# Optimization experiments

Measured on AMD Instinct MI355X. Metric: run time of the kernel, lower is better.

The kernel has to match this reference:

```python
import jax, jax.numpy as jnp
import numpy as np

NEI_SIZE = [16]  # matches init kwarg nei_size

def setup_inputs() -> dict:
    key = jax.random.key(0)
    k = jax.random.split(key, 5)
    B, N, S = 512, 32, 16
    EF, NF = 64, 128
    return {
        "x": jax.random.normal(k[0], (B, N, NF), dtype=jnp.float32),
        "x_nei_rel": jax.random.normal(k[1], (B, N * S, EF), dtype=jnp.float32),
        "x_nei_node": jax.random.normal(k[2], (B, N * S, NF), dtype=jnp.float32),
        "W1_w": jax.random.normal(k[3], (NF, EF + NF), dtype=jnp.float32) * 0.05,
        "W1_b": jax.random.normal(k[4], (NF,), dtype=jnp.float32) * 0.05,
        "i": 0,
    }

def reference(x, x_nei_rel, x_nei_node, W1_w, W1_b, i):
    S = NEI_SIZE[i]                       # now_nei_size (static python int)
    B, N, D = x.shape                     # N = n_neibor, D = nodeFea
    norm = 1.0 / np.sqrt(D).astype(np.float32)
    # concat edge+node feats and project: [B, N*S, EF+NF] -> [B, N*S, D]
    x_nei = jnp.concatenate([x_nei_rel, x_nei_node], axis=-1)
    v = (x_nei @ W1_w.T + W1_b).reshape(B, N, S, D)
    # per-node attention over its S neighbors
    alpha = jnp.einsum('bnd,bnsd->bns', x, v) * norm   # [B, N, S]
    alpha = jax.nn.softmax(alpha, axis=-1)
    # weighted neighbor sum
    return jnp.einsum('bns,bnsd->bnd', alpha, v)       # [B, N, D]
```

## Files before the change

### kernel.cpp

```cpp
#include <hip/hip_runtime.h>
#include <stdint.h>


typedef __attribute__((ext_vector_type(8))) short short8;
typedef __attribute__((ext_vector_type(4))) float float4_t;
typedef __attribute__((ext_vector_type(4))) unsigned short ushort4_t;

#define GRID_ 1024
#define ITERS_ 8

__device__ __forceinline__ unsigned short f2bf(float f) {
    uint32_t u = __float_as_uint(f);
    u += 0x7fffu + ((u >> 16) & 1u);
    return (unsigned short)(u >> 16);
}

__device__ __forceinline__ int aoff(int s, int kc) {
    return (((kc >> 5) * 64) + (((kc & 31) >> 3) * 16) + s) * 8 + (kc & 7);
}

__global__ __launch_bounds__(512, 8) void nei_attn_kernel(
    const float* __restrict__ x,
    const float* __restrict__ rel,
    const float* __restrict__ node,
    const float* __restrict__ W,
    const float* __restrict__ bias,
    float* __restrict__ out)
{
    __shared__ __align__(16) unsigned short lds_a[2][6 * 64 * 8];
    __shared__ float lds_x[2][128];
    __shared__ float lds_v[2][16 * 132];
    __shared__ float lds_alpha[2][16];

    const int t    = threadIdx.x;
    const int tl   = t & 255;
    const int h    = t >> 8;
    const int lane = t & 63;
    const int wv   = t >> 6;
    const int l15  = lane & 15;
    const int quad = (lane >> 4) & 3;

    short8 bf[6];
    const int row = wv * 16 + l15;
    const float bias_c = bias[row];
    #pragma unroll
    for (int q = 0; q < 6; ++q) {
        const float* p = W + row * 192 + q * 32 + quad * 8;
        float4_t a0 = *(const float4_t*)p;
        float4_t a1 = *(const float4_t*)(p + 4);
        short8 f;
        f[0] = (short)f2bf(a0.x); f[1] = (short)f2bf(a0.y);
        f[2] = (short)f2bf(a0.z); f[3] = (short)f2bf(a0.w);
        f[4] = (short)f2bf(a1.x); f[5] = (short)f2bf(a1.y);
        f[6] = (short)f2bf(a1.z); f[7] = (short)f2bf(a1.w);
        bf[q] = f;
    }

    const int s0 = tl >> 4,  kc0 = (tl & 15) << 2;
    const int s1 = tl >> 5,  kc1 = 64 + ((tl & 31) << 2);
    const int s2 = s1 + 8;
    const int ao0 = h * 3072 + aoff(s0, kc0);
    const int ao1 = h * 3072 + aoff(s1, kc1);
    const int ao2 = h * 3072 + aoff(s2, kc1);
    unsigned short* la = &lds_a[0][0];

    int idx = blockIdx.x * (ITERS_ * 2);

    float4_t pf0, pf1, pf2;
    float pfx = 0.f;
    {
        const float* pr = rel  + (idx + h) * 1024;
        const float* pn = node + (idx + h) * 2048;
        pf0 = *(const float4_t*)(pr + tl * 4);
        pf1 = *(const float4_t*)(pn + tl * 4);
        pf2 = *(const float4_t*)(pn + 1024 + tl * 4);
        if (t < 256) pfx = x[(idx + (t >> 7)) * 128 + (t & 127)];
    }

    for (int it = 0; it < ITERS_; ++it) {
        {
            ushort4_t u;
            u[0] = f2bf(pf0.x); u[1] = f2bf(pf0.y); u[2] = f2bf(pf0.z); u[3] = f2bf(pf0.w);
            *(ushort4_t*)&la[ao0] = u;
            u[0] = f2bf(pf1.x); u[1] = f2bf(pf1.y); u[2] = f2bf(pf1.z); u[3] = f2bf(pf1.w);
            *(ushort4_t*)&la[ao1] = u;
            u[0] = f2bf(pf2.x); u[1] = f2bf(pf2.y); u[2] = f2bf(pf2.z); u[3] = f2bf(pf2.w);
            *(ushort4_t*)&la[ao2] = u;
            if (t < 256) lds_x[t >> 7][t & 127] = pfx;
        }
        __syncthreads();

        if (it + 1 < ITERS_) {
            const int nidx = idx + 2;
            const float* pr = rel  + (nidx + h) * 1024;
            const float* pn = node + (nidx + h) * 2048;
            pf0 = *(const float4_t*)(pr + tl * 4);
            pf1 = *(const float4_t*)(pn + tl * 4);
            pf2 = *(const float4_t*)(pn + 1024 + tl * 4);
            if (t < 256) pfx = x[(nidx + (t >> 7)) * 128 + (t & 127)];
        }

        float4_t acc0 = {0.f, 0.f, 0.f, 0.f};
        float4_t acc1 = {0.f, 0.f, 0.f, 0.f};
        #pragma unroll
        for (int q = 0; q < 6; ++q) {
            short8 af0 = *(const short8*)&la[(q * 64 + lane) * 8];
            short8 af1 = *(const short8*)&la[3072 + (q * 64 + lane) * 8];
            acc0 = __builtin_amdgcn_mfma_f32_16x16x32_bf16(af0, bf[q], acc0, 0, 0, 0);
            acc1 = __builtin_amdgcn_mfma_f32_16x16x32_bf16(af1, bf[q], acc1, 0, 0, 0);
        }
        const int colw = wv * 16 + l15;
        const int rb = quad * 4;
        #pragma unroll
        for (int r = 0; r < 4; ++r) {
            lds_v[0][(rb + r) * 132 + colw] = acc0[r] + bias_c;
            lds_v[1][(rb + r) * 132 + colw] = acc1[r] + bias_c;
        }
        __syncthreads();

        {
            const int sA = tl >> 4, dA = tl & 15;
            float p = 0.f;
            #pragma unroll
            for (int j = 0; j < 8; ++j) {
                const int d = dA + (j << 4);
                p += lds_x[h][d] * lds_v[h][sA * 132 + d];
            }
            p += __shfl_xor(p, 8);
            p += __shfl_xor(p, 4);
            p += __shfl_xor(p, 2);
            p += __shfl_xor(p, 1);
            if (dA == 0) lds_alpha[h][sA] = p * 0.08838834764831845f;
        }
        __syncthreads();

        if (tl < 128) {
            const float* al = lds_alpha[h];
            float m = al[0];
            #pragma unroll
            for (int s = 1; s < 16; ++s) m = fmaxf(m, al[s]);
            float den = 0.f, o = 0.f;
            #pragma unroll
            for (int s = 0; s < 16; ++s) {
                const float e = __expf(al[s] - m);
                den += e;
                o += e * lds_v[h][s * 132 + tl];
            }
            out[(idx + h) * 128 + tl] = o / den;
        }
        idx += 2;
    }
}

extern "C" void kernel_launch(void* const* d_in, const int* in_sizes, int n_in,
                              void* d_out, int out_size, void* d_ws, size_t ws_size,
                              hipStream_t stream) {
    const float* x    = (const float*)d_in[0];
    const float* rel  = (const float*)d_in[1];
    const float* node = (const float*)d_in[2];
    const float* W    = (const float*)d_in[3];
    const float* bias = (const float*)d_in[4];
    float* out = (float*)d_out;
    hipLaunchKernelGGL(nei_attn_kernel, dim3(GRID_), dim3(512), 0, stream,
                       x, rel, node, W, bias, out);
}
```

Measured before the change: 305.6 us.

## Swizzle LDS A-tile layout, drop register prefetch, vectorize alpha dot reads

Applies an XOR swizzle to the bf16 A-tile layout in LDS, with matching index permutation on the MFMA fragment reads, to reduce bank conflicts on both the stores and the short8 loads. Removes the software prefetch of the next iteration's inputs into registers, so global loads now sit at the top of each iteration, and adds unroll 1 on the loop. This lowers register pressure at the cost of exposing global load latency, leaving overlap to other waves. The alpha dot product now reads contiguous 8-float runs per lane so the compiler can use vector LDS loads.

```diff
diff --git a/kernel.cpp b/kernel.cpp
--- a/kernel.cpp
+++ b/kernel.cpp
@@ -16,7 +16,9 @@
 }
 
 __device__ __forceinline__ int aoff(int s, int kc) {
-    return (((kc >> 5) * 64) + (((kc & 31) >> 3) * 16) + s) * 8 + (kc & 7);
+    int X = ((kc >> 5) << 6) + (((kc & 31) >> 3) << 4) + s;
+    X ^= ((X >> 3) ^ (X >> 6)) & 7;
+    return X * 8 + (kc & 7);
 }
 
 __global__ __launch_bounds__(512, 8) void nei_attn_kernel(
@@ -62,23 +64,19 @@
     const int ao0 = h * 3072 + aoff(s0, kc0);
     const int ao1 = h * 3072 + aoff(s1, kc1);
     const int ao2 = h * 3072 + aoff(s2, kc1);
+    const int lx = lane ^ ((lane >> 3) & 7);
     unsigned short* la = &lds_a[0][0];
 
     int idx = blockIdx.x * (ITERS_ * 2);
 
-    float4_t pf0, pf1, pf2;
-    float pfx = 0.f;
-    {
-        const float* pr = rel  + (idx + h) * 1024;
-        const float* pn = node + (idx + h) * 2048;
-        pf0 = *(const float4_t*)(pr + tl * 4);
-        pf1 = *(const float4_t*)(pn + tl * 4);
-        pf2 = *(const float4_t*)(pn + 1024 + tl * 4);
-        if (t < 256) pfx = x[(idx + (t >> 7)) * 128 + (t & 127)];
-    }
-
+    #pragma unroll 1
     for (int it = 0; it < ITERS_; ++it) {
         {
+            const float* pr = rel  + (idx + h) * 1024;
+            const float* pn = node + (idx + h) * 2048;
+            float4_t pf0 = *(const float4_t*)(pr + tl * 4);
+            float4_t pf1 = *(const float4_t*)(pn + tl * 4);
+            float4_t pf2 = *(const float4_t*)(pn + 1024 + tl * 4);
             ushort4_t u;
             u[0] = f2bf(pf0.x); u[1] = f2bf(pf0.y); u[2] = f2bf(pf0.z); u[3] = f2bf(pf0.w);
             *(ushort4_t*)&la[ao0] = u;
@@ -86,26 +84,16 @@
             *(ushort4_t*)&la[ao1] = u;
             u[0] = f2bf(pf2.x); u[1] = f2bf(pf2.y); u[2] = f2bf(pf2.z); u[3] = f2bf(pf2.w);
             *(ushort4_t*)&la[ao2] = u;
-            if (t < 256) lds_x[t >> 7][t & 127] = pfx;
+            if (t < 256) lds_x[t >> 7][t & 127] = x[(idx + (t >> 7)) * 128 + (t & 127)];
         }
         __syncthreads();
-
-        if (it + 1 < ITERS_) {
-            const int nidx = idx + 2;
-            const float* pr = rel  + (nidx + h) * 1024;
-            const float* pn = node + (nidx + h) * 2048;
-            pf0 = *(const float4_t*)(pr + tl * 4);
-            pf1 = *(const float4_t*)(pn + tl * 4);
-            pf2 = *(const float4_t*)(pn + 1024 + tl * 4);
-            if (t < 256) pfx = x[(nidx + (t >> 7)) * 128 + (t & 127)];
-        }
 
         float4_t acc0 = {0.f, 0.f, 0.f, 0.f};
         float4_t acc1 = {0.f, 0.f, 0.f, 0.f};
         #pragma unroll
         for (int q = 0; q < 6; ++q) {
-            short8 af0 = *(const short8*)&la[(q * 64 + lane) * 8];
-            short8 af1 = *(const short8*)&la[3072 + (q * 64 + lane) * 8];
+            short8 af0 = *(const short8*)&la[(q * 64 + (lx ^ q)) * 8];
+            short8 af1 = *(const short8*)&la[3072 + (q * 64 + (lx ^ q)) * 8];
             acc0 = __builtin_amdgcn_mfma_f32_16x16x32_bf16(af0, bf[q], acc0, 0, 0, 0);
             acc1 = __builtin_amdgcn_mfma_f32_16x16x32_bf16(af1, bf[q], acc1, 0, 0, 0);
         }
@@ -120,12 +108,11 @@
 
         {
             const int sA = tl >> 4, dA = tl & 15;
+            const float* vx = &lds_x[h][dA * 8];
+            const float* vv = &lds_v[h][sA * 132 + dA * 8];
             float p = 0.f;
             #pragma unroll
-            for (int j = 0; j < 8; ++j) {
-                const int d = dA + (j << 4);
-                p += lds_x[h][d] * lds_v[h][sA * 132 + d];
-            }
+            for (int j = 0; j < 8; ++j) p += vx[j] * vv[j];
             p += __shfl_xor(p, 8);
             p += __shfl_xor(p, 4);
             p += __shfl_xor(p, 2);
```

Result: faster. 285.8 us (-6.5%).

## Keep projected values in registers, swizzle LDS tiles, and halve per-block iterations

Applied to the files above, without the earlier changes.

The projected neighbor values are no longer written to LDS. The x-dot-v scores are now reduced with cross-lane shuffles plus a small per-wave partial-sum buffer, and the softmax-weighted sum is computed directly from the MFMA accumulators. The A-tile LDS layout gets an XOR swizzle to reduce bank conflicts on the fragment reads. The grid doubles while iterations per block halve, and the launch bounds occupancy hint drops from 8 to 6. Together these aim to cut LDS traffic and one large LDS round trip, at the cost of more shuffles and redundant exp work per lane.

```diff
diff --git a/kernel.cpp b/kernel.cpp
--- a/kernel.cpp
+++ b/kernel.cpp
@@ -6,8 +6,8 @@
 typedef __attribute__((ext_vector_type(4))) float float4_t;
 typedef __attribute__((ext_vector_type(4))) unsigned short ushort4_t;
 
-#define GRID_ 1024
-#define ITERS_ 8
+#define GRID_ 2048
+#define ITERS_ 4
 
 __device__ __forceinline__ unsigned short f2bf(float f) {
     uint32_t u = __float_as_uint(f);
@@ -16,10 +16,12 @@
 }
 
 __device__ __forceinline__ int aoff(int s, int kc) {
-    return (((kc >> 5) * 64) + (((kc & 31) >> 3) * 16) + s) * 8 + (kc & 7);
+    int X = ((kc >> 5) << 6) + (((kc & 31) >> 3) << 4) + s;
+    X ^= ((X >> 3) ^ (X >> 6)) & 7;
+    return X * 8 + (kc & 7);
 }
 
-__global__ __launch_bounds__(512, 8) void nei_attn_kernel(
+__global__ __launch_bounds__(512, 6) void nei_attn_kernel(
     const float* __restrict__ x,
     const float* __restrict__ rel,
     const float* __restrict__ node,
@@ -27,10 +29,9 @@
     const float* __restrict__ bias,
     float* __restrict__ out)
 {
-    __shared__ __align__(16) unsigned short lds_a[2][6 * 64 * 8];
-    __shared__ float lds_x[2][128];
-    __shared__ float lds_v[2][16 * 132];
-    __shared__ float lds_alpha[2][16];
+    __shared__ __align__(16) unsigned short lds_a[2][3072];
+    __shared__ __align__(16) float lds_ap[2][8][16];
+    __shared__ __align__(16) float lds_alpha[2][16];
 
     const int t    = threadIdx.x;
     const int tl   = t & 255;
@@ -39,13 +40,13 @@
     const int wv   = t >> 6;
     const int l15  = lane & 15;
     const int quad = (lane >> 4) & 3;
+    const int colw = wv * 16 + l15;
 
     short8 bf[6];
-    const int row = wv * 16 + l15;
-    const float bias_c = bias[row];
+    const float bias_c = bias[colw];
     #pragma unroll
     for (int q = 0; q < 6; ++q) {
-        const float* p = W + row * 192 + q * 32 + quad * 8;
+        const float* p = W + colw * 192 + q * 32 + quad * 8;
         float4_t a0 = *(const float4_t*)p;
         float4_t a1 = *(const float4_t*)(p + 4);
         short8 f;
@@ -62,21 +63,24 @@
     const int ao0 = h * 3072 + aoff(s0, kc0);
     const int ao1 = h * 3072 + aoff(s1, kc1);
     const int ao2 = h * 3072 + aoff(s2, kc1);
+    const int lx = lane ^ ((lane >> 3) & 7);
     unsigned short* la = &lds_a[0][0];
 
     int idx = blockIdx.x * (ITERS_ * 2);
 
     float4_t pf0, pf1, pf2;
-    float pfx = 0.f;
+    float px0, px1;
     {
         const float* pr = rel  + (idx + h) * 1024;
         const float* pn = node + (idx + h) * 2048;
         pf0 = *(const float4_t*)(pr + tl * 4);
         pf1 = *(const float4_t*)(pn + tl * 4);
         pf2 = *(const float4_t*)(pn + 1024 + tl * 4);
-        if (t < 256) pfx = x[(idx + (t >> 7)) * 128 + (t & 127)];
+        px0 = x[idx * 128 + colw];
+        px1 = x[(idx + 1) * 128 + colw];
     }
 
+    #pragma unroll 1
     for (int it = 0; it < ITERS_; ++it) {
         {
             ushort4_t u;
@@ -86,9 +90,10 @@
             *(ushort4_t*)&la[ao1] = u;
             u[0] = f2bf(pf2.x); u[1] = f2bf(pf2.y); u[2] = f2bf(pf2.z); u[3] = f2bf(pf2.w);
             *(ushort4_t*)&la[ao2] = u;
-            if (t < 256) lds_x[t >> 7][t & 127] = pfx;
         }
         __syncthreads();
+
+        const float cx0 = px0, cx1 = px1;
 
         if (it + 1 < ITERS_) {
             const int nidx = idx + 2;
@@ -97,57 +102,77 @@
             pf0 = *(const float4_t*)(pr + tl * 4);
             pf1 = *(const float4_t*)(pn + tl * 4);
             pf2 = *(const float4_t*)(pn + 1024 + tl * 4);
-            if (t < 256) pfx = x[(nidx + (t >> 7)) * 128 + (t & 127)];
+            px0 = x[nidx * 128 + colw];
+            px1 = x[(nidx + 1) * 128 + colw];
         }
 
         float4_t acc0 = {0.f, 0.f, 0.f, 0.f};
         float4_t acc1 = {0.f, 0.f, 0.f, 0.f};
         #pragma unroll
         for (int q = 0; q < 6; ++q) {
-            short8 af0 = *(const short8*)&la[(q * 64 + lane) * 8];
-            short8 af1 = *(const short8*)&la[3072 + (q * 64 + lane) * 8];
+            short8 af0 = *(const short8*)&la[(q * 64 + (lx ^ q)) * 8];
+            short8 af1 = *(const short8*)&la[3072 + (q * 64 + (lx ^ q)) * 8];
             acc0 = __builtin_amdgcn_mfma_f32_16x16x32_bf16(af0, bf[q], acc0, 0, 0, 0);
             acc1 = __builtin_amdgcn_mfma_f32_16x16x32_bf16(af1, bf[q], acc1, 0, 0, 0);
         }
-        const int colw = wv * 16 + l15;
-        const int rb = quad * 4;
         #pragma unroll
-        for (int r = 0; r < 4; ++r) {
-            lds_v[0][(rb + r) * 132 + colw] = acc0[r] + bias_c;
-            lds_v[1][(rb + r) * 132 + colw] = acc1[r] + bias_c;
+        for (int r = 0; r < 4; ++r) { acc0[r] += bias_c; acc1[r] += bias_c; }
+
+        float4_t pr0, pr1;
+        #pragma unroll
+        for (int r = 0; r < 4; ++r) { pr0[r] = cx0 * acc0[r]; pr1[r] = cx1 * acc1[r]; }
+        #pragma unroll
+        for (int msk = 1; msk <= 8; msk <<= 1) {
+            #pragma unroll
+            for (int r = 0; r < 4; ++r) {
+                pr0[r] += __shfl_xor(pr0[r], msk);
+                pr1[r] += __shfl_xor(pr1[r], msk);
+            }
+        }
+        if (l15 == 0) {
+            *(float4_t*)&lds_ap[0][wv][quad << 2] = pr0;
+            *(float4_t*)&lds_ap[1][wv][quad << 2] = pr1;
         }
         __syncthreads();
 
-        {
-            const int sA = tl >> 4, dA = tl & 15;
-            float p = 0.f;
+        if (t < 32) {
+            const int ht = t >> 4, s = t & 15;
+            float a = 0.f;
             #pragma unroll
-            for (int j = 0; j < 8; ++j) {
-                const int d = dA + (j << 4);
-                p += lds_x[h][d] * lds_v[h][sA * 132 + d];
-            }
-            p += __shfl_xor(p, 8);
-            p += __shfl_xor(p, 4);
-            p += __shfl_xor(p, 2);
-            p += __shfl_xor(p, 1);
-            if (dA == 0) lds_alpha[h][sA] = p * 0.08838834764831845f;
+            for (int w = 0; w < 8; ++w) a += lds_ap[ht][w][s];
+            lds_alpha[ht][s] = a * 0.08838834764831845f;
         }
         __syncthreads();
 
-        if (tl < 128) {
-            const float* al = lds_alpha[h];
-            float m = al[0];
-            #pragma unroll
-            for (int s = 1; s < 16; ++s) m = fmaxf(m, al[s]);
-            float den = 0.f, o = 0.f;
-            #pragma unroll
-            for (int s = 0; s < 16; ++s) {
-                const float e = __expf(al[s] - m);
-                den += e;
-                o += e * lds_v[h][s * 132 + tl];
-            }
-            out[(idx + h) * 128 + tl] = o / den;
+        #define SOFTMAX_TILE(AL, ACC, TIDX)                                         \
+        {                                                                           \
+            const float* al = (AL);                                                 \
+            float4_t a0 = *(const float4_t*)&al[0];                                 \
+            float4_t a1 = *(const float4_t*)&al[4];                                 \
+            float4_t a2 = *(const float4_t*)&al[8];                                 \
+            float4_t a3 = *(const float4_t*)&al[12];                                \
+            float4_t er = *(const float4_t*)&al[quad << 2];                         \
+            float mx = fmaxf(fmaxf(fmaxf(a0[0], a0[1]), fmaxf(a0[2], a0[3])),       \
+                             fmaxf(fmaxf(a1[0], a1[1]), fmaxf(a1[2], a1[3])));      \
+            mx = fmaxf(mx, fmaxf(fmaxf(fmaxf(a2[0], a2[1]), fmaxf(a2[2], a2[3])),   \
+                                 fmaxf(fmaxf(a3[0], a3[1]), fmaxf(a3[2], a3[3])))); \
+            float den = 0.f;                                                        \
+            _Pragma("unroll") for (int j = 0; j < 4; ++j) den += __expf(a0[j] - mx);\
+            _Pragma("unroll") for (int j = 0; j < 4; ++j) den += __expf(a1[j] - mx);\
+            _Pragma("unroll") for (int j = 0; j < 4; ++j) den += __expf(a2[j] - mx);\
+            _Pragma("unroll") for (int j = 0; j < 4; ++j) den += __expf(a3[j] - mx);\
+            float p = 0.f;                                                          \
+            _Pragma("unroll") for (int r = 0; r < 4; ++r)                           \
+                p += __expf(er[r] - mx) * (ACC)[r];                                 \
+            p += __shfl_xor(p, 16);                                                 \
+            p += __shfl_xor(p, 32);                                                 \
+            if (quad == 0) out[(TIDX) * 128 + colw] = p / den;                      \
         }
+
+        SOFTMAX_TILE(lds_alpha[0], acc0, idx)
+        SOFTMAX_TILE(lds_alpha[1], acc1, idx + 1)
+        #undef SOFTMAX_TILE
+
         idx += 2;
     }
 }
```

Result: no change. 305.5 us (-0.0%).
